# Kernel optimization log

Hardware: AMD Instinct MI355X
Metric: run time of the kernel (lower is better)

The kernel has to match this reference:

```python
import jax, jax.numpy as jnp
import numpy as np

B, T, D = 2, 2048, 2048
N, KH, H = 16, 8, 128  # query heads, kv heads, head_dim
S = 2048               # cache size
EPS = 1e-6
ROPE_THETA = 1000000.0
K_MASK = -0.7 * float(np.finfo(np.float32).max)  # jax _get_large_negative(float32)


def _rms_norm(x, w):
    rms = jnp.sqrt(jnp.mean(x.astype(jnp.float32) ** 2, axis=-1, keepdims=True) + EPS)
    return (w * x / rms).astype(x.dtype)


def _rope_embeddings(positions, head_dim):
    fraction = jnp.arange(0, head_dim, 2, dtype=jnp.float32) / head_dim
    inv_freq = 1.0 / (ROPE_THETA ** fraction)
    sinusoid = jnp.einsum('BT,k->BTk', positions.astype(jnp.float32), inv_freq,
                          precision=jax.lax.Precision.HIGHEST)
    return jnp.sin(sinusoid), jnp.cos(sinusoid)


def _apply_rope(x, sin, cos):
    h = x.shape[-1] // 2
    x1, x2 = x[..., :h], x[..., h:]
    s, c = sin[:, :, None, :], cos[:, :, None, :]
    return jnp.concatenate([x1 * c - x2 * s, x2 * c + x1 * s], axis=-1).astype(x.dtype)


def _positions_from_segment_ids(seg):
    t = seg.shape[1]
    pos = jnp.arange(t, dtype=jnp.int32)[None, :] - jnp.argmax(seg, axis=1)[:, None]
    return jnp.where(seg != 0, pos, 2 ** 30)


def _num_left_pad(seg):
    return jnp.sum(jnp.cumsum(seg != 0, axis=-1) == 0, axis=-1).astype(jnp.int32)


def _attention(x, q_w, k_w, v_w, o_w, q_norm_w, k_norm_w, k_cache, v_cache,
               segment_ids, start_ind, cur_ind):
    b, t, _ = x.shape
    s = k_cache.shape[1]
    n, kh, h = q_w.shape[1], k_w.shape[1], q_w.shape[2]

    q = _rms_norm(jnp.einsum('BTD,DNH->BTNH', x, q_w), q_norm_w)  # [B,T,N,H]
    k = _rms_norm(jnp.einsum('BSD,DKH->BSKH', x, k_w), k_norm_w)  # [B,T,K,H]
    v = jnp.einsum('BSD,DKH->BSKH', x, v_w)                       # [B,T,K,H]

    start = jnp.where(start_ind < 0, _num_left_pad(segment_ids), start_ind)
    pos = _positions_from_segment_ids(segment_ids) + cur_ind
    sin, cos = _rope_embeddings(pos, h)
    q = _apply_rope(q, sin, cos)
    k = _apply_rope(k, sin, cos)

    # KV-cache update at cur_ind
    k_cache = jax.lax.dynamic_update_slice(k_cache, k, (0, cur_ind, 0, 0))
    v_cache = jax.lax.dynamic_update_slice(v_cache, v, (0, cur_ind, 0, 0))

    # GQA: group query heads per kv head
    qg = q.reshape(b, t, kh, n // kh, h)
    logits = jnp.einsum('BTHGD,BSHD->BHGTS', qg, k_cache) * (h ** -0.5)

    q_pos = cur_ind + jnp.arange(t, dtype=jnp.int32)[None, :] - start[:, None]  # [B,T]
    ts = jnp.arange(s, dtype=jnp.int32)
    kv_seg = (ts[None, :] >= start[:, None]) & (ts[None, :] < cur_ind + t)      # [B,S] bool
    k_pos = ts[None, :] - start[:, None]                                        # [B,S]
    causal = k_pos[:, None, :] <= q_pos[:, :, None]                             # [B,T,S]
    # faithful to original: bool kv segment ids compared against int segment_ids
    seg_mask = kv_seg[:, None, :].astype(segment_ids.dtype) == segment_ids[:, :, None]
    final_mask = (causal & seg_mask)[:, None, None, :, :]                       # [B,1,1,T,S]

    logits = jnp.where(final_mask, logits, K_MASK)
    attn = jax.nn.softmax(logits.astype(jnp.float32), axis=-1).astype(logits.dtype)
    o = jnp.einsum('BHGTS,BSHD->BTHGD', attn, v_cache).reshape(b, t, n, h)
    return jnp.einsum('BTNH,NHD->BTD', o, o_w)


def setup_inputs() -> dict:
    key = jax.random.key(0)
    ks = jax.random.split(key, 5)
    scale = 0.02
    return {
        'x': jax.random.normal(ks[0], (B, T, D), jnp.float32),
        'q_w': jax.random.normal(ks[1], (D, N, H), jnp.float32) * scale,
        'k_w': jax.random.normal(ks[2], (D, KH, H), jnp.float32) * scale,
        'v_w': jax.random.normal(ks[3], (D, KH, H), jnp.float32) * scale,
        'o_w': jax.random.normal(ks[4], (N, H, D), jnp.float32) * scale,
        'q_norm_w': jnp.ones((H,), jnp.float32),
        'k_norm_w': jnp.ones((H,), jnp.float32),
        'k_cache': jnp.zeros((B, S, KH, H), jnp.float32),
        'v_cache': jnp.zeros((B, S, KH, H), jnp.float32),
        'segment_ids': jnp.ones((B, T), jnp.int32),
        'start_ind': jnp.zeros((B,), jnp.int32),
        'cur_ind': 0,
        'right_pads': 0,
    }


def reference(x, q_w, k_w, v_w, o_w, q_norm_w, k_norm_w, k_cache, v_cache,
              segment_ids, start_ind, cur_ind, right_pads):
    # right_pads only advances the cache write pointer (stateful side effect); it
    # does not affect the attention output.
    return _attention(x, q_w, k_w, v_w, o_w, q_norm_w, k_norm_w,
                      k_cache, v_cache, segment_ids, start_ind, cur_ind)
```

## Files before the change

kernel.cpp:

```cpp
#include <hip/hip_runtime.h>
#include <hip/hip_fp16.h>
#include <climits>
#include <math.h>

#define Bc   2
#define Tc   2048
#define Dc   2048
#define Nc   16
#define KHc  8
#define Hc   128
#define Sc   2048

constexpr float EPSc   = 1e-6f;
constexpr float SCALE2 = 0.1275174477984469f;

typedef short short8 __attribute__((ext_vector_type(8)));
typedef _Float16 half8 __attribute__((ext_vector_type(8)));
typedef __fp16 fp16x2 __attribute__((ext_vector_type(2)));
typedef float float4v __attribute__((ext_vector_type(4)));

union U16x8 { uint4 u; short8 s8; half8 h8; unsigned short us[8]; };
union H2U  { fp16x2 h; unsigned u; };
union S8H8 { short8 s; half8 h; };

__device__ __forceinline__ unsigned short f2bf(float f) {
    union { float f; unsigned u; } v; v.f = f;
    unsigned r = v.u + 0x7FFFu + ((v.u >> 16) & 1u);
    return (unsigned short)(r >> 16);
}
__device__ __forceinline__ float bf2f(unsigned short u) {
    union { unsigned u; float f; } v; v.u = ((unsigned)u) << 16;
    return v.f;
}

__device__ __forceinline__ void tc_body(const float* __restrict__ in,
                                        unsigned short* __restrict__ out,
                                        int R, int C, int bx, int by, int tid,
                                        float tile[32][33])
{
    int c0 = bx * 32, r0 = by * 32;
#pragma unroll
    for (int i = 0; i < 4; ++i) {
        int row = (tid >> 5) + i * 8, col = tid & 31;
        tile[row][col] = in[(size_t)(r0 + row) * C + c0 + col];
    }
    __syncthreads();
#pragma unroll
    for (int i = 0; i < 4; ++i) {
        int rowo = (tid >> 5) + i * 8, colo = tid & 31;
        out[(size_t)(c0 + rowo) * R + r0 + colo] = f2bf(tile[colo][rowo]);
    }
}

__global__ __launch_bounds__(256) void prep(const float* __restrict__ x,
                                            const float* __restrict__ qw,
                                            const float* __restrict__ kw,
                                            const float* __restrict__ vw,
                                            const float* __restrict__ ow,
                                            const int* __restrict__ seg,
                                            const int* __restrict__ start_ind,
                                            int* __restrict__ meta,
                                            unsigned short* __restrict__ xb,
                                            unsigned short* __restrict__ qkvwT,
                                            unsigned short* __restrict__ owT)
{
    __shared__ float tile[32][33];
    __shared__ int s_max, s_amax, s_nz;
    int id = blockIdx.x;
    int tid = threadIdx.x;

    if (id < Bc) {
        int b = id;
        if (tid == 0) { s_max = INT_MIN; s_amax = Tc; s_nz = Tc; }
        __syncthreads();
        int lmax = INT_MIN;
        for (int t = tid; t < Tc; t += 256) lmax = max(lmax, seg[b * Tc + t]);
        atomicMax(&s_max, lmax);
        __syncthreads();
        int mv = s_max;
        int lamax = Tc, lnz = Tc;
        for (int t = tid; t < Tc; t += 256) {
            int v = seg[b * Tc + t];
            if (v == mv) lamax = min(lamax, t);
            if (v != 0)  lnz   = min(lnz, t);
        }
        atomicMin(&s_amax, lamax);
        atomicMin(&s_nz, lnz);
        __syncthreads();
        if (tid == 0) {
            meta[b] = s_amax;
            int st = start_ind[b];
            meta[Bc + b] = (st < 0) ? s_nz : st;
        }
        return;
    }
    id -= Bc;
    if (id < 4096) {
        size_t base = ((size_t)id * 256 + tid) * 8;
        float4 a = *(const float4*)&x[base];
        float4 b = *(const float4*)&x[base + 4];
        U16x8 o;
        o.us[0] = f2bf(a.x); o.us[1] = f2bf(a.y); o.us[2] = f2bf(a.z); o.us[3] = f2bf(a.w);
        o.us[4] = f2bf(b.x); o.us[5] = f2bf(b.y); o.us[6] = f2bf(b.z); o.us[7] = f2bf(b.w);
        *(uint4*)&xb[base] = o.u;
        return;
    }
    id -= 4096;
    if (id < 4096) { tc_body(qw, qkvwT, 2048, 2048, id & 63, id >> 6, tid, tile); return; }
    id -= 4096;
    if (id < 2048) { tc_body(kw, qkvwT + (size_t)2048 * 2048, 2048, 1024, id & 31, id >> 5, tid, tile); return; }
    id -= 2048;
    if (id < 2048) { tc_body(vw, qkvwT + (size_t)3072 * 2048, 2048, 1024, id & 31, id >> 5, tid, tile); return; }
    id -= 2048;
    tc_body(ow, owT, 2048, 2048, id & 63, id >> 6, tid, tile);
}

__global__ __launch_bounds__(256, 2) void gemm_mfma(const unsigned short* __restrict__ A,
                                                    const unsigned short* __restrict__ BT,
                                                    void* __restrict__ Cout,
                                                    int M, int N, int K, int out_fp32)
{
    __shared__ __align__(16) unsigned short As[128 * 32];
    __shared__ __align__(16) unsigned short Bs[128 * 32];
    int tid = threadIdx.x;
    int lane = tid & 63, w = tid >> 6;
    int quad = lane >> 4, l15 = lane & 15;
    int bm = blockIdx.y * 128, bn = blockIdx.x * 128;
    int wm = (w >> 1) * 64, wn = (w & 1) * 64;

    int srow = lane >> 2;
    int pl   = lane & 3;
    int sw   = (quad ^ ((l15 >> 1) & 3)) * 8;

    float4v acc[16];
#pragma unroll
    for (int i = 0; i < 16; ++i) acc[i] = (float4v)0.f;

    for (int k0 = 0; k0 < K; k0 += 32) {
        __syncthreads();
#pragma unroll
        for (int c = 0; c < 2; ++c) {
            int j = w * 2 + c;
            int row = j * 16 + srow;
            int pg = pl ^ ((row >> 1) & 3);
            __builtin_amdgcn_global_load_lds(
                (__attribute__((address_space(1))) void*)(A + (size_t)(bm + row) * K + k0 + pg * 8),
                (__attribute__((address_space(3))) void*)(As + j * 512), 16, 0, 0);
            __builtin_amdgcn_global_load_lds(
                (__attribute__((address_space(1))) void*)(BT + (size_t)(bn + row) * K + k0 + pg * 8),
                (__attribute__((address_space(3))) void*)(Bs + j * 512), 16, 0, 0);
        }
        __syncthreads();
        short8 af[4];
#pragma unroll
        for (int mi = 0; mi < 4; ++mi)
            af[mi] = *(const short8*)&As[(wm + mi * 16 + l15) * 32 + sw];
#pragma unroll
        for (int ni = 0; ni < 4; ++ni) {
            short8 bf = *(const short8*)&Bs[(wn + ni * 16 + l15) * 32 + sw];
#pragma unroll
            for (int mi = 0; mi < 4; ++mi)
                acc[mi * 4 + ni] = __builtin_amdgcn_mfma_f32_16x16x32_bf16(af[mi], bf, acc[mi * 4 + ni], 0, 0, 0);
        }
    }

#pragma unroll
    for (int mi = 0; mi < 4; ++mi)
#pragma unroll
        for (int ni = 0; ni < 4; ++ni)
#pragma unroll
            for (int reg = 0; reg < 4; ++reg) {
                int row = bm + wm + mi * 16 + quad * 4 + reg;
                int col = bn + wn + ni * 16 + l15;
                float v = acc[mi * 4 + ni][reg];
                if (out_fp32) ((float*)Cout)[(size_t)row * N + col] = v;
                else ((unsigned short*)Cout)[(size_t)row * N + col] = f2bf(v);
            }
}

__global__ __launch_bounds__(256) void post(unsigned short* __restrict__ QKVh,
                                            unsigned short* __restrict__ Kall,
                                            unsigned short* __restrict__ Vt,
                                            const float* __restrict__ qw,
                                            const float* __restrict__ kw,
                                            const int* __restrict__ seg,
                                            const int* __restrict__ meta,
                                            const int* __restrict__ cur_ptr,
                                            const float* __restrict__ kc,
                                            const float* __restrict__ vc)
{
    int id = blockIdx.x;
    int tid = threadIdx.x;
    int cur = cur_ptr[0];

    if (id < 24576) {
        int rowid = id * 4 + (tid >> 6);
        int lane = tid & 63;
        int hh = rowid % 24;
        int bt = rowid / 24;
        int t = bt & (Tc - 1);
        int b = bt >> 11;

        const unsigned short* in;
        unsigned short* out;
        const float* wt;
        if (hh < 16) {
            unsigned short* p = QKVh + (size_t)bt * 4096 + hh * Hc;
            in = p; out = p; wt = qw;
        } else {
            int kh = hh - 16;
            in = QKVh + (size_t)bt * 4096 + 2048 + kh * Hc;
            out = Kall + (((size_t)b * Sc + cur + t) * KHc + kh) * Hc;
            wt = kw;
        }
        float v1 = bf2f(in[lane]), v2 = bf2f(in[lane + 64]);
        float ssq = v1 * v1 + v2 * v2;
#pragma unroll
        for (int off = 1; off < 64; off <<= 1) ssq += __shfl_xor(ssq, off);
        float rinv = rsqrtf(ssq * (1.0f / Hc) + EPSc);

        int sg = seg[bt];
        long long pos = (sg != 0) ? (long long)(t - meta[b]) : (long long)(1 << 30);
        float posf = (float)(pos + (long long)cur);
        float inv_freq = exp2f(-(float)lane * (19.931568569324174f / 64.0f));
        float s, c;
        sincosf(posf * inv_freq, &s, &c);

        float n1 = wt[lane] * v1 * rinv;
        float n2 = wt[lane + 64] * v2 * rinv;
        out[lane]      = f2bf(n1 * c - n2 * s);
        out[lane + 64] = f2bf(n2 * c + n1 * s);
        return;
    }
    id -= 24576;
    if (id < 2048) {
        size_t base = ((size_t)id * 256 + tid) * 8;
        int s = (int)((base >> 10) & (Sc - 1));
        if (s >= cur && s < cur + Tc) return;
        float4 a = *(const float4*)&kc[base];
        float4 b = *(const float4*)&kc[base + 4];
        U16x8 o;
        o.us[0] = f2bf(a.x); o.us[1] = f2bf(a.y); o.us[2] = f2bf(a.z); o.us[3] = f2bf(a.w);
        o.us[4] = f2bf(b.x); o.us[5] = f2bf(b.y); o.us[6] = f2bf(b.z); o.us[7] = f2bf(b.w);
        *(uint4*)&Kall[base] = o.u;
        return;
    }
    id -= 2048;
    {
        int gid = id * 256 + tid;
        int h  = gid & 127;
        int s8 = ((gid >> 7) & 255) * 8;
        int kh = (gid >> 15) & 7;
        int b  = gid >> 18;
        int curT = cur + Tc;
        unsigned short tmp[8];
#pragma unroll
        for (int e = 0; e < 8; ++e) {
            int s = s8 + e;
            float f;
            if (s >= cur && s < curT)
                f = bf2f(QKVh[(size_t)(b * Tc + (s - cur)) * 4096 + 3072 + kh * Hc + h]);
            else
                f = vc[((size_t)(b * Sc + s) * KHc + kh) * Hc + h];
            tmp[e] = __half_as_ushort(__float2half(f));
        }
        *(uint4*)&Vt[(((size_t)b * KHc + kh) * Hc + h) * Sc + s8] = *(uint4*)tmp;
    }
}

__global__ __launch_bounds__(512, 4) void flash_mfma(const unsigned short* __restrict__ Qb,
                                                     const unsigned short* __restrict__ Kall,
                                                     const unsigned short* __restrict__ Vt,
                                                     const int* __restrict__ seg,
                                                     const int* __restrict__ meta,
                                                     const int* __restrict__ cur_ptr,
                                                     unsigned short* __restrict__ Ob)
{
    __shared__ __align__(16) unsigned short Ks[64 * 128];
    __shared__ __align__(16) unsigned short Vs[128 * 64];
    __shared__ __align__(16) unsigned short Ps[128 * 64];

    int tid = threadIdx.x;
    int lane = tid & 63, w = tid >> 6;
    int quad = lane >> 4, l15 = lane & 15;
    int bid = blockIdx.x;
    int raw = bid & 15;
    int n  = (bid >> 4) & 15;
    int b  = bid >> 8;
    int qt = (b == 0) ? raw : (15 - raw);
    int kh = n >> 1;
    int cur = cur_ptr[0];
    int startb = meta[Bc + b];
    int curT = cur + Tc;
    int t0 = qt * 128 + w * 16;

    short8 qf[4];
#pragma unroll
    for (int ks = 0; ks < 4; ++ks) {
        int row = t0 + l15;
        U16x8 uq;
        uq.u = *(const uint4*)&Qb[(size_t)(b * Tc + row) * 4096 + n * Hc + ks * 32 + quad * 8];
        qf[ks] = uq.s8;
    }

    int trow0 = t0 + l15;
    int sg0 = seg[b * Tc + trow0];
    int cls = (sg0 == 0) ? 0 : ((sg0 == 1) ? 1 : 2);
    int ct  = cur + trow0;
    unsigned long long mball = __ballot(cls == 1);
    bool allseg1 = (mball == 0xFFFFFFFFFFFFFFFFull);

    float lsum = 0.f;
    float4v oT[8];
#pragma unroll
    for (int i = 0; i < 8; ++i) oT[i] = (float4v)0.f;

    int s_end = min(Sc, cur + qt * 128 + 128);
    int nch = (s_end + 63) >> 6;

    const size_t kstride = (size_t)KHc * Hc;
    const unsigned short* kptr[2];
    unsigned short* kdst[2];
#pragma unroll
    for (int i = 0; i < 2; ++i) {
        int j = w * 2 + i;
        int row = j * 4 + (lane >> 4);
        int pl = lane & 15;
        int pg = pl ^ ((row >> 1) & 7);
        kptr[i] = Kall + (size_t)b * Sc * kstride + (size_t)row * kstride + kh * Hc + pg * 8;
        kdst[i] = Ks + j * 512;
    }
    const unsigned short* vptr[2];
    unsigned short* vdst[2];
#pragma unroll
    for (int i = 0; i < 2; ++i) {
        int j = w * 2 + i;
        int h = j * 8 + (lane >> 3);
        int pl = lane & 7;
        int pg = pl ^ ((h >> 1) & 7);
        vptr[i] = Vt + ((size_t)b * KHc + kh) * (size_t)Hc * Sc + (size_t)h * Sc + pg * 8;
        vdst[i] = Vs + j * 512;
    }
    int sw3 = (l15 >> 1) & 7;
    int sw8 = l15 & 7;
    unsigned short* psrow = Ps + (w * 16 + l15) * 64;

    for (int c = 0; c < nch; ++c) {
        int s0 = c * 64;
#pragma unroll
        for (int i = 0; i < 2; ++i) {
            __builtin_amdgcn_global_load_lds(
                (__attribute__((address_space(1))) void*)(kptr[i] + (size_t)s0 * kstride),
                (__attribute__((address_space(3))) void*)kdst[i], 16, 0, 0);
            __builtin_amdgcn_global_load_lds(
                (__attribute__((address_space(1))) void*)(vptr[i] + s0),
                (__attribute__((address_space(3))) void*)vdst[i], 16, 0, 0);
        }
        __syncthreads();

        float4v st[4];
#pragma unroll
        for (int i = 0; i < 4; ++i) st[i] = (float4v)0.f;
        __builtin_amdgcn_s_setprio(1);
#pragma unroll
        for (int ks = 0; ks < 4; ++ks) {
#pragma unroll
            for (int stile = 0; stile < 4; ++stile) {
                short8 kf = *(const short8*)&Ks[(stile * 16 + l15) * 128 + ((ks * 4 + quad) ^ sw3) * 8];
                st[stile] = __builtin_amdgcn_mfma_f32_16x16x32_bf16(kf, qf[ks], st[stile], 0, 0, 0);
            }
        }
        __builtin_amdgcn_s_setprio(0);

        bool fullok = allseg1 && (s0 >= startb) && (s0 + 63 <= cur + t0) && (s0 + 63 < curT);

#pragma unroll
        for (int stile = 0; stile < 4; ++stile) {
            float p0, p1, p2, p3;
            if (fullok) {
                p0 = exp2f(st[stile][0] * SCALE2);
                p1 = exp2f(st[stile][1] * SCALE2);
                p2 = exp2f(st[stile][2] * SCALE2);
                p3 = exp2f(st[stile][3] * SCALE2);
            } else {
                float pp[4];
#pragma unroll
                for (int reg = 0; reg < 4; ++reg) {
                    int s = s0 + stile * 16 + quad * 4 + reg;
                    int kvseg = (s >= startb && s < curT) ? 1 : 0;
                    bool ok = (s <= ct) && (cls == kvseg);
                    pp[reg] = exp2f(ok ? st[stile][reg] * SCALE2 : -1e30f);
                }
                p0 = pp[0]; p1 = pp[1]; p2 = pp[2]; p3 = pp[3];
            }
            lsum += (p0 + p1) + (p2 + p3);
            H2U a, d;
            a.h = __builtin_amdgcn_cvt_pkrtz(p0, p1);
            d.h = __builtin_amdgcn_cvt_pkrtz(p2, p3);
            uint2 pk; pk.x = a.u; pk.y = d.u;
            *(uint2*)&psrow[(((stile * 2 + (quad >> 1)) ^ sw8) << 3) + (quad & 1) * 4] = pk;
        }

        __builtin_amdgcn_s_setprio(1);
#pragma unroll
        for (int kk = 0; kk < 2; ++kk) {
            S8H8 pf;
            pf.s = *(const short8*)&psrow[((kk * 4 + quad) ^ sw8) << 3];
#pragma unroll
            for (int htile = 0; htile < 8; ++htile) {
                S8H8 vf;
                vf.s = *(const short8*)&Vs[(htile * 16 + l15) * 64 + ((kk * 4 + quad) ^ sw3) * 8];
                oT[htile] = __builtin_amdgcn_mfma_f32_16x16x32_f16(vf.h, pf.h, oT[htile], 0, 0, 0);
            }
        }
        __builtin_amdgcn_s_setprio(0);

        __syncthreads();
    }

    float l = lsum;
    l += __shfl_xor(l, 16);
    l += __shfl_xor(l, 32);
    float linv = (l > 0.f) ? (1.0f / l) : 0.f;

    {
        int trow = t0 + l15;
        size_t base = ((size_t)(b * Tc + trow) * Nc + n) * Hc;
#pragma unroll
        for (int htile = 0; htile < 8; ++htile) {
            float4v v = oT[htile];
            unsigned short r0 = f2bf(v[0] * linv);
            unsigned short r1 = f2bf(v[1] * linv);
            unsigned short r2 = f2bf(v[2] * linv);
            unsigned short r3 = f2bf(v[3] * linv);
            uint2 pk;
            pk.x = (unsigned)r0 | ((unsigned)r1 << 16);
            pk.y = (unsigned)r2 | ((unsigned)r3 << 16);
            *(uint2*)&Ob[base + htile * 16 + quad * 4] = pk;
        }
    }
}

extern "C" void kernel_launch(void* const* d_in, const int* in_sizes, int n_in,
                              void* d_out, int out_size, void* d_ws, size_t ws_size,
                              hipStream_t stream)
{
    const float* x        = (const float*)d_in[0];
    const float* q_w      = (const float*)d_in[1];
    const float* k_w      = (const float*)d_in[2];
    const float* v_w      = (const float*)d_in[3];
    const float* o_w      = (const float*)d_in[4];
    const float* q_norm_w = (const float*)d_in[5];
    const float* k_norm_w = (const float*)d_in[6];
    const float* k_cache  = (const float*)d_in[7];
    const float* v_cache  = (const float*)d_in[8];
    const int*   seg      = (const int*)d_in[9];
    const int*   startind = (const int*)d_in[10];
    const int*   cur_ptr  = (const int*)d_in[11];
    (void)in_sizes; (void)n_in; (void)out_size; (void)ws_size;

    char* base = (char*)d_ws;
    int* meta = (int*)base;
    unsigned short* QKVh = (unsigned short*)(base + 1024);
    unsigned short* Kall = (unsigned short*)(base + 33555456);
    unsigned short* Vt   = (unsigned short*)(base + 41944064);
    unsigned short* xb   = (unsigned short*)(base + 50332672);
    unsigned short* qkvwT= (unsigned short*)(base + 67109888);
    unsigned short* owT  = (unsigned short*)(base + 83887104);
    unsigned short* Ob   = xb;

    prep<<<Bc + 4096 + 4096 + 2048 + 2048 + 4096, 256, 0, stream>>>(
        x, q_w, k_w, v_w, o_w, seg, startind, meta, xb, qkvwT, owT);

    gemm_mfma<<<dim3(32, 32), 256, 0, stream>>>(xb, qkvwT, QKVh, Bc * Tc, 4096, Dc, 0);

    post<<<24576 + 2048 + 2048, 256, 0, stream>>>(QKVh, Kall, Vt,
        q_norm_w, k_norm_w, seg, meta, cur_ptr, k_cache, v_cache);

    flash_mfma<<<Bc * Nc * (Tc / 128), 512, 0, stream>>>(QKVh, Kall, Vt, seg, meta, cur_ptr, Ob);

    gemm_mfma<<<dim3(16, 32), 256, 0, stream>>>(Ob, owT, d_out, Bc * Tc, Dc, Nc * Hc, 1);
}
```

Before: 379.1 us.

## Replace 128x128 GEMM with double-buffered 256x256 pipelined MFMA kernel

Replaces the 128x128-tile, single-buffer GEMM with a 256x256-tile, 512-thread kernel that uses K-step 64 and double-buffered LDS. Global-to-LDS loads for the next tiles are interleaved with MFMA quarters, using explicit barriers, waitcnt and setprio. It also adds an XCD-aware workgroup swizzle and an XOR-swizzled LDS layout. This aims to hide load latency and raise arithmetic intensity, but the large LDS footprint and tiles give fewer workgroups (128 for the output projection), which risks under-filling the GPU.

```diff
diff --git a/kernel.cpp b/kernel.cpp
--- a/kernel.cpp
+++ b/kernel.cpp
@@ -115,64 +115,188 @@
     tc_body(ow, owT, 2048, 2048, id & 63, id >> 6, tid, tile);
 }
 
-__global__ __launch_bounds__(256, 2) void gemm_mfma(const unsigned short* __restrict__ A,
-                                                    const unsigned short* __restrict__ BT,
-                                                    void* __restrict__ Cout,
-                                                    int M, int N, int K, int out_fp32)
+#define GSYNC_IN()  do { asm volatile("" ::: "memory"); \
+                         __builtin_amdgcn_s_barrier(); \
+                         asm volatile("s_waitcnt lgkmcnt(0)" ::: "memory"); \
+                         __builtin_amdgcn_sched_barrier(0); \
+                         __builtin_amdgcn_s_setprio(1); } while (0)
+#define GSYNC_OUT() do { __builtin_amdgcn_s_setprio(0); \
+                         __builtin_amdgcn_sched_barrier(0); \
+                         asm volatile("" ::: "memory"); \
+                         __builtin_amdgcn_s_barrier(); } while (0)
+#define GSYNC_OUT_KT() do { __builtin_amdgcn_s_setprio(0); \
+                         __builtin_amdgcn_sched_barrier(0); \
+                         asm volatile("s_waitcnt vmcnt(4)" ::: "memory"); \
+                         __builtin_amdgcn_s_barrier(); \
+                         asm volatile("" ::: "memory"); } while (0)
+
+__global__ __launch_bounds__(512, 2) void gemm256(const unsigned short* __restrict__ A,
+                                                  const unsigned short* __restrict__ BT,
+                                                  void* __restrict__ Cout,
+                                                  int M, int N, int K, int out_fp32)
 {
-    __shared__ __align__(16) unsigned short As[128 * 32];
-    __shared__ __align__(16) unsigned short Bs[128 * 32];
+    __shared__ __align__(16) unsigned short As[2 * 16384];
+    __shared__ __align__(16) unsigned short Bs[2 * 16384];
+
     int tid = threadIdx.x;
     int lane = tid & 63, w = tid >> 6;
     int quad = lane >> 4, l15 = lane & 15;
-    int bm = blockIdx.y * 128, bn = blockIdx.x * 128;
-    int wm = (w >> 1) * 64, wn = (w & 1) * 64;
-
-    int srow = lane >> 2;
-    int pl   = lane & 3;
-    int sw   = (quad ^ ((l15 >> 1) & 3)) * 8;
-
-    float4v acc[16];
-#pragma unroll
-    for (int i = 0; i < 16; ++i) acc[i] = (float4v)0.f;
-
-    for (int k0 = 0; k0 < K; k0 += 32) {
-        __syncthreads();
-#pragma unroll
-        for (int c = 0; c < 2; ++c) {
-            int j = w * 2 + c;
-            int row = j * 16 + srow;
-            int pg = pl ^ ((row >> 1) & 3);
-            __builtin_amdgcn_global_load_lds(
-                (__attribute__((address_space(1))) void*)(A + (size_t)(bm + row) * K + k0 + pg * 8),
-                (__attribute__((address_space(3))) void*)(As + j * 512), 16, 0, 0);
-            __builtin_amdgcn_global_load_lds(
-                (__attribute__((address_space(1))) void*)(BT + (size_t)(bn + row) * K + k0 + pg * 8),
-                (__attribute__((address_space(3))) void*)(Bs + j * 512), 16, 0, 0);
-        }
-        __syncthreads();
-        short8 af[4];
-#pragma unroll
-        for (int mi = 0; mi < 4; ++mi)
-            af[mi] = *(const short8*)&As[(wm + mi * 16 + l15) * 32 + sw];
-#pragma unroll
-        for (int ni = 0; ni < 4; ++ni) {
-            short8 bf = *(const short8*)&Bs[(wn + ni * 16 + l15) * 32 + sw];
+
+    int gx = gridDim.x;
+    int nwg = gx * gridDim.y;
+    int lin = blockIdx.y * gx + blockIdx.x;
+    int swz = (lin & 7) * (nwg >> 3) + (lin >> 3);
+    int bm = (swz / gx) * 256, bn = (swz % gx) * 256;
+
+    int KT = K >> 6;
+
+    int colswz = (((lane & 7) ^ ((lane >> 3) & 7)) << 3);
+    int r0 = (w * 2) * 8 + (lane >> 3);
+    int r1 = (w * 2 + 1) * 8 + (lane >> 3);
+    const unsigned short* Ab0 = A + (size_t)(bm + r0) * K + colswz;
+    const unsigned short* Ab1 = A + (size_t)(bm + r1) * K + colswz;
+    const unsigned short* Bb0 = BT + (size_t)(bn + r0) * K + colswz;
+    const unsigned short* Bb1 = BT + (size_t)(bn + r1) * K + colswz;
+    size_t hK = (size_t)128 * K;
+
+    unsigned short* dA0 = As + (w * 2) * 512;
+    unsigned short* dA1 = As + (w * 2 + 1) * 512;
+    unsigned short* dB0 = Bs + (w * 2) * 512;
+    unsigned short* dB1 = Bs + (w * 2 + 1) * 512;
+
+    auto stA = [&](int kt, int h, int bufp) __attribute__((always_inline)) {
+        __builtin_amdgcn_global_load_lds(
+            (__attribute__((address_space(1))) void*)(Ab0 + h * hK + (size_t)kt * 64),
+            (__attribute__((address_space(3))) void*)(dA0 + bufp * 16384 + h * 8192), 16, 0, 0);
+        __builtin_amdgcn_global_load_lds(
+            (__attribute__((address_space(1))) void*)(Ab1 + h * hK + (size_t)kt * 64),
+            (__attribute__((address_space(3))) void*)(dA1 + bufp * 16384 + h * 8192), 16, 0, 0);
+    };
+    auto stB = [&](int kt, int h, int bufp) __attribute__((always_inline)) {
+        __builtin_amdgcn_global_load_lds(
+            (__attribute__((address_space(1))) void*)(Bb0 + h * hK + (size_t)kt * 64),
+            (__attribute__((address_space(3))) void*)(dB0 + bufp * 16384 + h * 8192), 16, 0, 0);
+        __builtin_amdgcn_global_load_lds(
+            (__attribute__((address_space(1))) void*)(Bb1 + h * hK + (size_t)kt * 64),
+            (__attribute__((address_space(3))) void*)(dB1 + bufp * 16384 + h * 8192), 16, 0, 0);
+    };
+
+    int ards = (w >> 2) * 8192;
+    int brds = (w & 3) * 4096;
+    int rowb = l15 * 64;
+    int swA = l15 & 7;
+    int cof0 = ((quad) ^ swA) << 3;
+    int cof1 = ((4 + quad) ^ swA) << 3;
+
+    float4v acc[8][4];
+#pragma unroll
+    for (int i = 0; i < 8; ++i)
+#pragma unroll
+        for (int j = 0; j < 4; ++j) acc[i][j] = (float4v)0.f;
+
+    stA(0, 0, 0); stA(0, 1, 0); stB(0, 0, 0); stB(0, 1, 0);
+    stA(1, 0, 1); stA(1, 1, 1);
+    asm volatile("s_waitcnt vmcnt(4)" ::: "memory");
+    __builtin_amdgcn_s_barrier();
+    asm volatile("" ::: "memory");
+
+    auto ktile = [&](int kt, int bufp) __attribute__((always_inline)) {
+        bool sB = (kt + 1) < KT;
+        bool sA = (kt + 2) < KT;
+        const unsigned short* ab = As + bufp * 16384 + ards + rowb;
+        const unsigned short* bb = Bs + bufp * 16384 + brds + rowb;
+        short8 afl[2][4], afh[2][4], bfa[2][2], bfb[2][2];
+
+#pragma unroll
+        for (int mi = 0; mi < 4; ++mi) {
+            afl[0][mi] = *(const short8*)&ab[mi * 1024 + cof0];
+            afl[1][mi] = *(const short8*)&ab[mi * 1024 + cof1];
+        }
+#pragma unroll
+        for (int ni = 0; ni < 2; ++ni) {
+            bfa[0][ni] = *(const short8*)&bb[ni * 1024 + cof0];
+            bfa[1][ni] = *(const short8*)&bb[ni * 1024 + cof1];
+        }
+        if (sB) stB(kt + 1, 0, bufp ^ 1);
+        GSYNC_IN();
+#pragma unroll
+        for (int kk = 0; kk < 2; ++kk)
 #pragma unroll
             for (int mi = 0; mi < 4; ++mi)
-                acc[mi * 4 + ni] = __builtin_amdgcn_mfma_f32_16x16x32_bf16(af[mi], bf, acc[mi * 4 + ni], 0, 0, 0);
-        }
-    }
-
-#pragma unroll
-    for (int mi = 0; mi < 4; ++mi)
+#pragma unroll
+                for (int ni = 0; ni < 2; ++ni)
+                    acc[mi][ni] = __builtin_amdgcn_mfma_f32_16x16x32_bf16(afl[kk][mi], bfa[kk][ni], acc[mi][ni], 0, 0, 0);
+        GSYNC_OUT();
+
+#pragma unroll
+        for (int mi = 0; mi < 4; ++mi) {
+            afh[0][mi] = *(const short8*)&ab[(4 + mi) * 1024 + cof0];
+            afh[1][mi] = *(const short8*)&ab[(4 + mi) * 1024 + cof1];
+        }
+#pragma unroll
+        for (int ni = 0; ni < 2; ++ni) {
+            bfb[0][ni] = *(const short8*)&bb[(2 + ni) * 1024 + cof0];
+            bfb[1][ni] = *(const short8*)&bb[(2 + ni) * 1024 + cof1];
+        }
+        if (sB) stB(kt + 1, 1, bufp ^ 1);
+        GSYNC_IN();
+#pragma unroll
+        for (int kk = 0; kk < 2; ++kk)
+#pragma unroll
+            for (int mi = 0; mi < 4; ++mi)
+#pragma unroll
+                for (int ni = 0; ni < 2; ++ni)
+                    acc[mi][2 + ni] = __builtin_amdgcn_mfma_f32_16x16x32_bf16(afl[kk][mi], bfb[kk][ni], acc[mi][2 + ni], 0, 0, 0);
+        GSYNC_OUT();
+
+#pragma unroll
+        for (int ni = 0; ni < 2; ++ni) {
+            bfa[0][ni] = *(const short8*)&bb[ni * 1024 + cof0];
+            bfa[1][ni] = *(const short8*)&bb[ni * 1024 + cof1];
+        }
+        if (sA) stA(kt + 2, 0, bufp);
+        GSYNC_IN();
+#pragma unroll
+        for (int kk = 0; kk < 2; ++kk)
+#pragma unroll
+            for (int mi = 0; mi < 4; ++mi)
+#pragma unroll
+                for (int ni = 0; ni < 2; ++ni)
+                    acc[4 + mi][ni] = __builtin_amdgcn_mfma_f32_16x16x32_bf16(afh[kk][mi], bfa[kk][ni], acc[4 + mi][ni], 0, 0, 0);
+        GSYNC_OUT();
+
+#pragma unroll
+        for (int ni = 0; ni < 2; ++ni) {
+            bfb[0][ni] = *(const short8*)&bb[(2 + ni) * 1024 + cof0];
+            bfb[1][ni] = *(const short8*)&bb[(2 + ni) * 1024 + cof1];
+        }
+        if (sA) stA(kt + 2, 1, bufp);
+        GSYNC_IN();
+#pragma unroll
+        for (int kk = 0; kk < 2; ++kk)
+#pragma unroll
+            for (int mi = 0; mi < 4; ++mi)
+#pragma unroll
+                for (int ni = 0; ni < 2; ++ni)
+                    acc[4 + mi][2 + ni] = __builtin_amdgcn_mfma_f32_16x16x32_bf16(afh[kk][mi], bfb[kk][ni], acc[4 + mi][2 + ni], 0, 0, 0);
+        GSYNC_OUT_KT();
+    };
+
+    for (int kt = 0; kt < KT; kt += 2) {
+        ktile(kt, 0);
+        ktile(kt + 1, 1);
+    }
+
+    int wm = (w >> 2) * 128, wn = (w & 3) * 64;
+#pragma unroll
+    for (int mi = 0; mi < 8; ++mi)
 #pragma unroll
         for (int ni = 0; ni < 4; ++ni)
 #pragma unroll
             for (int reg = 0; reg < 4; ++reg) {
                 int row = bm + wm + mi * 16 + quad * 4 + reg;
                 int col = bn + wn + ni * 16 + l15;
-                float v = acc[mi * 4 + ni][reg];
+                float v = acc[mi][ni][reg];
                 if (out_fp32) ((float*)Cout)[(size_t)row * N + col] = v;
                 else ((unsigned short*)Cout)[(size_t)row * N + col] = f2bf(v);
             }
@@ -472,12 +596,12 @@
     prep<<<Bc + 4096 + 4096 + 2048 + 2048 + 4096, 256, 0, stream>>>(
         x, q_w, k_w, v_w, o_w, seg, startind, meta, xb, qkvwT, owT);
 
-    gemm_mfma<<<dim3(32, 32), 256, 0, stream>>>(xb, qkvwT, QKVh, Bc * Tc, 4096, Dc, 0);
+    gemm256<<<dim3(16, 16), 512, 0, stream>>>(xb, qkvwT, QKVh, Bc * Tc, 4096, Dc, 0);
 
     post<<<24576 + 2048 + 2048, 256, 0, stream>>>(QKVh, Kall, Vt,
         q_norm_w, k_norm_w, seg, meta, cur_ptr, k_cache, v_cache);
 
     flash_mfma<<<Bc * Nc * (Tc / 128), 512, 0, stream>>>(QKVh, Kall, Vt, seg, meta, cur_ptr, Ob);
 
-    gemm_mfma<<<dim3(16, 32), 256, 0, stream>>>(Ob, owT, d_out, Bc * Tc, Dc, Nc * Hc, 1);
-}
+    gemm256<<<dim3(8, 16), 512, 0, stream>>>(Ob, owT, d_out, Bc * Tc, Dc, Nc * Hc, 1);
+}
```

After: 393.0 us. 1.04x slower.
